# Kernel tuning notes

Measured on AMD Instinct MI355X. Metric: run time of the kernel, lower is better.

Reference implementation:

```python
import jax, jax.numpy as jnp
import numpy as np

B, L, E, H, NB, WIN = 128, 512, 512, 8, 2, 64
HD = E // H
EPS = 1e-8


def setup_inputs() -> dict:
    key = jax.random.key(0)
    ks = jax.random.split(key, 10)
    s = 0.02
    return {
        "timeline_mask": jax.random.randint(ks[0], (B, L), 0, 10) == 0,
        "seqs": jax.random.normal(ks[1], (B, L, E), jnp.float32),
        "w_in": jax.random.normal(ks[2], (NB, 3 * E, E), jnp.float32) * s,
        "b_in": jnp.zeros((NB, 3 * E), jnp.float32),
        "w_out": jax.random.normal(ks[3], (NB, E, E), jnp.float32) * s,
        "b_out": jnp.zeros((NB, E), jnp.float32),
        "ln1_g": jnp.ones((NB, E), jnp.float32),
        "ln1_b": jnp.zeros((NB, E), jnp.float32),
        "ln2_g": jnp.ones((NB, E), jnp.float32),
        "ln2_b": jnp.zeros((NB, E), jnp.float32),
        "c1_w": jax.random.normal(ks[4], (NB, E, E), jnp.float32) * s,
        "c1_b": jnp.zeros((NB, E), jnp.float32),
        "c2_w": jax.random.normal(ks[5], (NB, E, E), jnp.float32) * s,
        "c2_b": jnp.zeros((NB, E), jnp.float32),
        "lnf_g": jnp.ones((E,), jnp.float32),
        "lnf_b": jnp.zeros((E,), jnp.float32),
    }


def _ln(x, g, b):
    m = x.mean(-1, keepdims=True)
    v = ((x - m) ** 2).mean(-1, keepdims=True)
    return (x - m) * jax.lax.rsqrt(v + EPS) * g + b


def reference(timeline_mask, seqs, w_in, b_in, w_out, b_out,
              ln1_g, ln1_b, ln2_g, ln2_b, c1_w, c1_b, c2_w, c2_b,
              lnf_g, lnf_b):
    i = jnp.arange(L)
    d = i[:, None] - i[None, :]
    allowed = (d >= 0) & (d < WIN)  # [L, L] bool, True = attend

    keep = (~timeline_mask)[..., None].astype(seqs.dtype)  # [B, L, 1]
    x = seqs * keep
    scale = 1.0 / np.sqrt(HD)
    neg = jnp.asarray(jnp.finfo(seqs.dtype).min, seqs.dtype)

    for blk in range(NB):
        q_in = _ln(x, ln1_g[blk], ln1_b[blk])  # torch: query = LN(seqs), key/value = raw seqs
        wq, wk, wv = jnp.split(w_in[blk], 3, axis=0)
        bq, bk, bv = jnp.split(b_in[blk], 3, axis=0)
        q = (q_in @ wq.T + bq).reshape(B, L, H, HD)
        k = (x @ wk.T + bk).reshape(B, L, H, HD)
        v = (x @ wv.T + bv).reshape(B, L, H, HD)
        scores = jnp.einsum("blhd,bmhd->bhlm", q, k) * scale
        scores = jnp.where(allowed, scores, neg)
        attn = jax.nn.softmax(scores, axis=-1)
        o = jnp.einsum("bhlm,bmhd->blhd", attn, v).reshape(B, L, E)
        o = o @ w_out[blk].T + b_out[blk]
        x = q_in + o  # residual onto the layernormed query, as in the original
        x = _ln(x, ln2_g[blk], ln2_b[blk])
        h = jax.nn.relu(x @ c1_w[blk].T + c1_b[blk])  # Conv1d k=1 == pointwise linear
        x = (h @ c2_w[blk].T + c2_b[blk]) + x
        x = x * keep

    return _ln(x, lnf_g, lnf_b)
```

## Files before the change

### kernel.cpp

```cpp
#include <hip/hip_runtime.h>
#include <cstdint>

#define B_   128
#define L_   512
#define E_   512
#define H_   8
#define HD_  64
#define NB_  2
#define WIN_ 64
#define NROW (B_ * L_)

typedef __attribute__((ext_vector_type(8))) __bf16 bf16x8;
typedef __attribute__((ext_vector_type(4))) float f32x4;

static __device__ __forceinline__ unsigned short f2bf(float f) {
  union { float f; unsigned int u; } c; c.f = f;
  unsigned int u = c.u;
  unsigned int r = (u + 0x7fffu + ((u >> 16) & 1u)) >> 16;
  return (unsigned short)r;
}
static __device__ __forceinline__ float bf2f(unsigned short s) {
  union { unsigned int u; float f; } c; c.u = ((unsigned int)s) << 16; return c.f;
}

static __device__ __forceinline__ void gld_lds16(const unsigned short* g, unsigned short* l) {
  __builtin_amdgcn_global_load_lds((const __attribute__((address_space(1))) void*)g,
                                   (__attribute__((address_space(3))) void*)l, 16, 0, 0);
}

__global__ void detect_mask_kernel(const unsigned char* tm, int* flag) {
  __shared__ int f;
  if (threadIdx.x == 0) f = 0;
  __syncthreads();
  int local = 0;
  for (int i = threadIdx.x; i < NROW; i += blockDim.x)
    if ((i & 3) && tm[i]) local = 1;
  if (local) atomicOr(&f, 1);
  __syncthreads();
  if (threadIdx.x == 0) *flag = f;
}

__global__ void expand_keep_kernel(const void* tmv, const int* flag, float* keepF) {
  int i = blockIdx.x * blockDim.x + threadIdx.x;
  if (i >= NROW) return;
  int m;
  if (*flag) m = ((const unsigned char*)tmv)[i] != 0;
  else       m = ((const int*)tmv)[i] != 0;
  keepF[i] = m ? 0.f : 1.f;
}

__global__ void f2bf_kernel(const float* __restrict__ in, unsigned short* __restrict__ out, int n) {
  int i = blockIdx.x * blockDim.x + threadIdx.x;
  if (i < n) out[i] = f2bf(in[i]);
}

__global__ void mask_kernel(const float* __restrict__ seqs, const float* __restrict__ keepF,
                            unsigned short* __restrict__ xB) {
  int i = blockIdx.x * blockDim.x + threadIdx.x;
  int idx = i * 4;
  int row = idx >> 9;
  float k = keepF[row];
  float4 v = *(const float4*)(seqs + idx);
  ushort4 b;
  b.x = f2bf(v.x * k); b.y = f2bf(v.y * k); b.z = f2bf(v.z * k); b.w = f2bf(v.w * k);
  *(ushort4*)(xB + idx) = b;
}

__global__ __launch_bounds__(256) void ln_kernel(const unsigned short* __restrict__ X,
                                                 const float* __restrict__ g,
                                                 const float* __restrict__ bb,
                                                 unsigned short* outB, float* outF) {
  int wave = threadIdx.x >> 6, lane = threadIdx.x & 63;
  size_t row = (size_t)blockIdx.x * 4 + wave;
  const unsigned short* xr = X + row * E_;
  int e0 = lane * 8;
  union { uint4 q; unsigned short s[8]; } raw;
  raw.q = *(const uint4*)(xr + e0);
  float v[8];
#pragma unroll
  for (int i = 0; i < 8; ++i) v[i] = bf2f(raw.s[i]);
  float s = 0.f, s2 = 0.f;
#pragma unroll
  for (int i = 0; i < 8; ++i) { s += v[i]; s2 += v[i] * v[i]; }
  for (int off = 32; off; off >>= 1) { s += __shfl_xor(s, off); s2 += __shfl_xor(s2, off); }
  float mean = s * (1.f / E_);
  float var  = s2 * (1.f / E_) - mean * mean;
  float rs = rsqrtf(var + 1e-8f);
  float4 g0 = *(const float4*)(g + e0),  g1 = *(const float4*)(g + e0 + 4);
  float4 b0 = *(const float4*)(bb + e0), b1 = *(const float4*)(bb + e0 + 4);
  float gg[8] = {g0.x, g0.y, g0.z, g0.w, g1.x, g1.y, g1.z, g1.w};
  float bv[8] = {b0.x, b0.y, b0.z, b0.w, b1.x, b1.y, b1.z, b1.w};
  float y[8];
#pragma unroll
  for (int i = 0; i < 8; ++i) y[i] = (v[i] - mean) * rs * gg[i] + bv[i];
  if (outB) {
    union { uint4 q; unsigned short s[8]; } pk;
#pragma unroll
    for (int i = 0; i < 8; ++i) pk.s[i] = f2bf(y[i]);
    *(uint4*)(outB + row * E_ + e0) = pk.q;
  }
  if (outF) {
    float4 y0 = {y[0], y[1], y[2], y[3]}, y1 = {y[4], y[5], y[6], y[7]};
    *(float4*)(outF + row * E_ + e0) = y0;
    *(float4*)(outF + row * E_ + e0 + 4) = y1;
  }
}

__global__ __launch_bounds__(256) void gemm_kernel(
    const unsigned short* __restrict__ A, const unsigned short* __restrict__ W,
    const float* __restrict__ bias, const unsigned short* res, const float* __restrict__ keepF,
    unsigned short* outB, int K, int M, int relu) {
  __shared__ unsigned short sA0[128 * 32];
  __shared__ unsigned short sA1[128 * 32];
  __shared__ unsigned short sW0[128 * 32];
  __shared__ unsigned short sW1[128 * 32];
  int tid = threadIdx.x;
  int wave = tid >> 6, lane = tid & 63;
  int lm = lane & 15, quad = lane >> 4;
  size_t row0 = (size_t)blockIdx.y * 128;
  int col0 = blockIdx.x * 128;
  int wm = (wave >> 1) * 64, wn = (wave & 1) * 64;

  f32x4 acc[4][4];
  f32x4 z = {0.f, 0.f, 0.f, 0.f};
#pragma unroll
  for (int i = 0; i < 4; ++i)
#pragma unroll
    for (int j = 0; j < 4; ++j) acc[i][j] = z;

  int ar0 = tid >> 2, ak0 = (tid & 3) * 8;
  int ar1 = ar0 + 64;
  unsigned short* dA0a = &sA0[(wave * 16) * 32];
  unsigned short* dA0b = &sA0[(wave * 16 + 64) * 32];
  unsigned short* dA1a = &sA1[(wave * 16) * 32];
  unsigned short* dA1b = &sA1[(wave * 16 + 64) * 32];
  unsigned short* dW0a = &sW0[(wave * 16) * 32];
  unsigned short* dW0b = &sW0[(wave * 16 + 64) * 32];
  unsigned short* dW1a = &sW1[(wave * 16) * 32];
  unsigned short* dW1b = &sW1[(wave * 16 + 64) * 32];
  const unsigned short* Ar0 = A + (row0 + ar0) * K + ak0;
  const unsigned short* Ar1 = A + (row0 + ar1) * K + ak0;
  const unsigned short* Wr0 = W + (size_t)(col0 + ar0) * K + ak0;
  const unsigned short* Wr1 = W + (size_t)(col0 + ar1) * K + ak0;

  for (int k0 = 0; k0 < K; k0 += 64) {
    __syncthreads();
    gld_lds16(Ar0 + k0,      dA0a);
    gld_lds16(Ar1 + k0,      dA0b);
    gld_lds16(Ar0 + k0 + 32, dA1a);
    gld_lds16(Ar1 + k0 + 32, dA1b);
    gld_lds16(Wr0 + k0,      dW0a);
    gld_lds16(Wr1 + k0,      dW0b);
    gld_lds16(Wr0 + k0 + 32, dW1a);
    gld_lds16(Wr1 + k0 + 32, dW1b);
    __syncthreads();
    bf16x8 a0[4], a1[4], b0[4], b1[4];
#pragma unroll
    for (int mt = 0; mt < 4; ++mt) {
      a0[mt] = *(const bf16x8*)&sA0[(wm + mt * 16 + lm) * 32 + quad * 8];
      a1[mt] = *(const bf16x8*)&sA1[(wm + mt * 16 + lm) * 32 + quad * 8];
    }
#pragma unroll
    for (int nt = 0; nt < 4; ++nt) {
      b0[nt] = *(const bf16x8*)&sW0[(wn + nt * 16 + lm) * 32 + quad * 8];
      b1[nt] = *(const bf16x8*)&sW1[(wn + nt * 16 + lm) * 32 + quad * 8];
    }
#pragma unroll
    for (int mt = 0; mt < 4; ++mt)
#pragma unroll
      for (int nt = 0; nt < 4; ++nt) {
        acc[mt][nt] = __builtin_amdgcn_mfma_f32_16x16x32_bf16(a0[mt], b0[nt], acc[mt][nt], 0, 0, 0);
        acc[mt][nt] = __builtin_amdgcn_mfma_f32_16x16x32_bf16(a1[mt], b1[nt], acc[mt][nt], 0, 0, 0);
      }
  }

#pragma unroll
  for (int mt = 0; mt < 4; ++mt) {
#pragma unroll
    for (int r = 0; r < 4; ++r) {
      size_t row = row0 + wm + mt * 16 + quad * 4 + r;
      float kf = keepF ? keepF[row] : 1.f;
#pragma unroll
      for (int nt = 0; nt < 4; ++nt) {
        int col = col0 + wn + nt * 16 + lm;
        float v = acc[mt][nt][r] + bias[col];
        if (res) v += bf2f(res[row * M + col]);
        if (relu) v = fmaxf(v, 0.f);
        v *= kf;
        outB[row * M + col] = f2bf(v);
      }
    }
  }
}

#define SQS 72
#define SKS 72
#define SVS 68
#define SPS 136
__global__ __launch_bounds__(256) void attn_kernel(const unsigned short* __restrict__ Q,
                                                   const unsigned short* __restrict__ K,
                                                   const unsigned short* __restrict__ V,
                                                   unsigned short* O) {
  __shared__ unsigned short smem[64 * SQS + 128 * SKS + 128 * SVS];
  unsigned short* sQ = smem;
  unsigned short* sK = smem + 64 * SQS;
  unsigned short* sV = smem + 64 * SQS + 128 * SKS;
  unsigned short* sP = smem;

  int i0 = blockIdx.x * 64;
  int h = blockIdx.y;
  int b = blockIdx.z;
  int tid = threadIdx.x;
  size_t qbase  = ((size_t)b * L_) * E_ + h * HD_;
  size_t kvbase = ((size_t)b * L_) * (2 * E_) + h * HD_;

  for (int f = tid; f < 512; f += 256) {
    int r = f >> 3, c = f & 7;
    uint4 v = *(const uint4*)&Q[qbase + (size_t)(i0 + r) * E_ + c * 8];
    *(uint4*)&sQ[r * SQS + c * 8] = v;
  }
  for (int f = tid; f < 1024; f += 256) {
    int r = f >> 3, c = f & 7;
    int j = i0 - 64 + r;
    uint4 v = {0, 0, 0, 0};
    if (j >= 0) v = *(const uint4*)&K[kvbase + (size_t)j * (2 * E_) + c * 8];
    *(uint4*)&sK[r * SKS + c * 8] = v;
  }
  for (int f = tid; f < 2048; f += 256) {
    int r = f >> 4, c = f & 15;
    int j = i0 - 64 + r;
    uint2 v = {0, 0};
    if (j >= 0) v = *(const uint2*)&V[kvbase + E_ + (size_t)j * (2 * E_) + c * 4];
    *(uint2*)&sV[r * SVS + c * 4] = v;
  }
  __syncthreads();

  int wave = tid >> 6, lane = tid & 63;
  int lm = lane & 15, quad = lane >> 4;
  int wq = wave * 16;

  f32x4 accs[8];
  f32x4 z4 = {0.f, 0.f, 0.f, 0.f};
#pragma unroll
  for (int nt = 0; nt < 8; ++nt) accs[nt] = z4;
  bf16x8 aq0 = *(const bf16x8*)&sQ[(wq + lm) * SQS + quad * 8];
  bf16x8 aq1 = *(const bf16x8*)&sQ[(wq + lm) * SQS + 32 + quad * 8];
#pragma unroll
  for (int nt = 0; nt < 8; ++nt) {
    bf16x8 bk0 = *(const bf16x8*)&sK[(nt * 16 + lm) * SKS + quad * 8];
    bf16x8 bk1 = *(const bf16x8*)&sK[(nt * 16 + lm) * SKS + 32 + quad * 8];
    accs[nt] = __builtin_amdgcn_mfma_f32_16x16x32_bf16(aq0, bk0, accs[nt], 0, 0, 0);
    accs[nt] = __builtin_amdgcn_mfma_f32_16x16x32_bf16(aq1, bk1, accs[nt], 0, 0, 0);
  }
  __syncthreads();

#pragma unroll
  for (int r = 0; r < 4; ++r) {
    int qi = wq + quad * 4 + r;
    float sv[8];
    float mx = -INFINITY;
#pragma unroll
    for (int nt = 0; nt < 8; ++nt) {
      int jn = nt * 16 + lm;
      int d = qi + 64 - jn;
      int j = i0 - 64 + jn;
      float s = (d >= 0 && d < WIN_ && j >= 0) ? accs[nt][r] * 0.125f : -INFINITY;
      sv[nt] = s;
      mx = fmaxf(mx, s);
    }
#pragma unroll
    for (int off = 1; off <= 8; off <<= 1) mx = fmaxf(mx, __shfl_xor(mx, off));
    float sum = 0.f;
#pragma unroll
    for (int nt = 0; nt < 8; ++nt) {
      float e = __expf(sv[nt] - mx);
      sv[nt] = e;
      sum += e;
    }
#pragma unroll
    for (int off = 1; off <= 8; off <<= 1) sum += __shfl_xor(sum, off);
    float inv = 1.f / sum;
#pragma unroll
    for (int nt = 0; nt < 8; ++nt) accs[nt][r] = sv[nt] * inv;
  }

#pragma unroll
  for (int nt = 0; nt < 8; ++nt)
#pragma unroll
    for (int r = 0; r < 4; ++r)
      sP[(wq + quad * 4 + r) * SPS + nt * 16 + lm] = f2bf(accs[nt][r]);
  __syncthreads();

  f32x4 acco[4];
#pragma unroll
  for (int nt = 0; nt < 4; ++nt) acco[nt] = z4;
#pragma unroll
  for (int kt = 0; kt < 4; ++kt) {
    bf16x8 ap = *(const bf16x8*)&sP[(wq + lm) * SPS + kt * 32 + quad * 8];
    int jb = kt * 32 + quad * 8;
#pragma unroll
    for (int nt = 0; nt < 4; ++nt) {
      union { unsigned short u[8]; bf16x8 v; } bv;
#pragma unroll
      for (int jj = 0; jj < 8; ++jj)
        bv.u[jj] = sV[(jb + jj) * SVS + nt * 16 + lm];
      acco[nt] = __builtin_amdgcn_mfma_f32_16x16x32_bf16(ap, bv.v, acco[nt], 0, 0, 0);
    }
  }
#pragma unroll
  for (int nt = 0; nt < 4; ++nt)
#pragma unroll
    for (int r = 0; r < 4; ++r) {
      int qi = wq + quad * 4 + r;
      O[qbase + (size_t)(i0 + qi) * E_ + nt * 16 + lm] = f2bf(acco[nt][r]);
    }
}

extern "C" void kernel_launch(void* const* d_in, const int* in_sizes, int n_in,
                              void* d_out, int out_size, void* d_ws, size_t ws_size,
                              hipStream_t stream) {
  const void*  tm    = d_in[0];
  const float* seqs  = (const float*)d_in[1];
  const float* w_in  = (const float*)d_in[2];
  const float* b_in  = (const float*)d_in[3];
  const float* w_out = (const float*)d_in[4];
  const float* b_out = (const float*)d_in[5];
  const float* ln1_g = (const float*)d_in[6];
  const float* ln1_b = (const float*)d_in[7];
  const float* ln2_g = (const float*)d_in[8];
  const float* ln2_b = (const float*)d_in[9];
  const float* c1_w  = (const float*)d_in[10];
  const float* c1_b  = (const float*)d_in[11];
  const float* c2_w  = (const float*)d_in[12];
  const float* c2_b  = (const float*)d_in[13];
  const float* lnf_g = (const float*)d_in[14];
  const float* lnf_b = (const float*)d_in[15];

  char* ws = (char*)d_ws;
  size_t off = 0;
  auto alloc = [&](size_t bytes) -> char* {
    char* p = ws + off;
    off += (bytes + 255) & ~(size_t)255;
    return p;
  };
  const size_t NE = (size_t)NROW * E_;
  unsigned short* xb     = (unsigned short*)alloc(NE * 2);
  unsigned short* qinb   = (unsigned short*)alloc(NE * 2);
  unsigned short* qb     = (unsigned short*)alloc(NE * 2);
  unsigned short* kvb    = (unsigned short*)alloc(NE * 4);
  unsigned short* w_in_b = (unsigned short*)alloc((size_t)NB_ * 3 * E_ * E_ * 2);
  unsigned short* w_out_b= (unsigned short*)alloc((size_t)NB_ * E_ * E_ * 2);
  unsigned short* wc1b   = (unsigned short*)alloc((size_t)NB_ * E_ * E_ * 2);
  unsigned short* wc2b   = (unsigned short*)alloc((size_t)NB_ * E_ * E_ * 2);
  float*          keepF  = (float*)alloc((size_t)NROW * 4);
  int*            flag   = (int*)alloc(256);
  if (off > ws_size) return;

  unsigned short* hb = kvb;

  detect_mask_kernel<<<1, 256, 0, stream>>>((const unsigned char*)tm, flag);
  expand_keep_kernel<<<NROW / 256, 256, 0, stream>>>(tm, flag, keepF);

  int n_win = NB_ * 3 * E_ * E_, n_sq = NB_ * E_ * E_;
  f2bf_kernel<<<(n_win + 255) / 256, 256, 0, stream>>>(w_in, w_in_b, n_win);
  f2bf_kernel<<<(n_sq + 255) / 256, 256, 0, stream>>>(w_out, w_out_b, n_sq);
  f2bf_kernel<<<(n_sq + 255) / 256, 256, 0, stream>>>(c1_w, wc1b, n_sq);
  f2bf_kernel<<<(n_sq + 255) / 256, 256, 0, stream>>>(c2_w, wc2b, n_sq);

  mask_kernel<<<(int)(NE / 4 / 256), 256, 0, stream>>>(seqs, keepF, xb);

  dim3 ggrid(E_ / 128, NROW / 128);
  dim3 ggridKV(2 * E_ / 128, NROW / 128);
  for (int blk = 0; blk < NB_; ++blk) {
    const unsigned short* wq = w_in_b + (size_t)blk * 3 * E_ * E_;
    const unsigned short* wkv = wq + (size_t)E_ * E_;
    const float* bq = b_in + (size_t)blk * 3 * E_;
    const float* bkv = bq + E_;

    ln_kernel<<<NROW / 4, 256, 0, stream>>>(xb, ln1_g + blk * E_, ln1_b + blk * E_, qinb, nullptr);
    gemm_kernel<<<ggrid, 256, 0, stream>>>(qinb, wq, bq, nullptr, nullptr, qb, E_, E_, 0);
    gemm_kernel<<<ggridKV, 256, 0, stream>>>(xb, wkv, bkv, nullptr, nullptr, kvb, E_, 2 * E_, 0);
    attn_kernel<<<dim3(L_ / 64, H_, B_), 256, 0, stream>>>(qb, kvb, kvb, qb);
    gemm_kernel<<<ggrid, 256, 0, stream>>>(qb, w_out_b + (size_t)blk * E_ * E_,
                                           b_out + blk * E_, qinb, nullptr, xb, E_, E_, 0);
    ln_kernel<<<NROW / 4, 256, 0, stream>>>(xb, ln2_g + blk * E_, ln2_b + blk * E_, xb, nullptr);
    gemm_kernel<<<ggrid, 256, 0, stream>>>(xb, wc1b + (size_t)blk * E_ * E_,
                                           c1_b + blk * E_, nullptr, nullptr, hb, E_, E_, 1);
    gemm_kernel<<<ggrid, 256, 0, stream>>>(hb, wc2b + (size_t)blk * E_ * E_,
                                           c2_b + blk * E_, xb, keepF, xb, E_, E_, 0);
  }
  ln_kernel<<<NROW / 4, 256, 0, stream>>>(xb, lnf_g, lnf_b, nullptr, (float*)d_out);
}
```

Baseline: 1.630 ms.

## Fold layernorms into GEMMs, double-buffer GEMM, banded attention with transposed V

Replaces the LN1/LN2 materialising kernels with per-row stats kernels. Gamma is folded into bf16 weights and the mean/rstd correction into the GEMM epilogue through precomputed U/C vectors, and the LN'd residual is recomputed from stats in the epilogue. The GEMM gets double-buffered LDS staging with one barrier per k-step and an XCD-aware block remap. Attention now skips key tiles outside the sliding-window band and stores V transposed in LDS so B-operand loads are vectorised. The risks are doubled LDS in the GEMM, which may lower occupancy, slight numeric drift from folding LN after bf16 rounding, and removal of a barrier between the sP writes and reads in attention.

```diff
diff --git a/kernel.cpp b/kernel.cpp
--- a/kernel.cpp
+++ b/kernel.cpp
@@ -54,6 +54,24 @@
   if (i < n) out[i] = f2bf(in[i]);
 }
 
+__global__ void f2bf_scale_kernel(const float* __restrict__ in, const float* __restrict__ g,
+                                  unsigned short* __restrict__ out, int n) {
+  int i = blockIdx.x * blockDim.x + threadIdx.x;
+  if (i < n) out[i] = f2bf(in[i] * g[i & (E_ - 1)]);
+}
+
+__global__ __launch_bounds__(256) void uc_kernel(const float* __restrict__ W, const float* __restrict__ g,
+                                                 const float* __restrict__ b, const float* __restrict__ bias,
+                                                 float* __restrict__ U, float* __restrict__ C) {
+  int wave = threadIdx.x >> 6, lane = threadIdx.x & 63;
+  int j = blockIdx.x * 4 + wave;
+  const float* wr = W + (size_t)j * E_;
+  float su = 0.f, sc = 0.f;
+  for (int k = lane; k < E_; k += 64) { float w = wr[k]; su += w * g[k]; sc += w * b[k]; }
+  for (int off = 32; off; off >>= 1) { su += __shfl_xor(su, off); sc += __shfl_xor(sc, off); }
+  if (lane == 0) { U[j] = su; C[j] = sc + bias[j]; }
+}
+
 __global__ void mask_kernel(const float* __restrict__ seqs, const float* __restrict__ keepF,
                             unsigned short* __restrict__ xB) {
   int i = blockIdx.x * blockDim.x + threadIdx.x;
@@ -64,6 +82,24 @@
   ushort4 b;
   b.x = f2bf(v.x * k); b.y = f2bf(v.y * k); b.z = f2bf(v.z * k); b.w = f2bf(v.w * k);
   *(ushort4*)(xB + idx) = b;
+}
+
+__global__ __launch_bounds__(256) void stats_kernel(const unsigned short* __restrict__ X,
+                                                    float* __restrict__ st) {
+  int wave = threadIdx.x >> 6, lane = threadIdx.x & 63;
+  size_t row = (size_t)blockIdx.x * 4 + wave;
+  union { uint4 q; unsigned short s[8]; } raw;
+  raw.q = *(const uint4*)(X + row * E_ + lane * 8);
+  float s = 0.f, s2 = 0.f;
+#pragma unroll
+  for (int i = 0; i < 8; ++i) { float v = bf2f(raw.s[i]); s += v; s2 += v * v; }
+  for (int off = 32; off; off >>= 1) { s += __shfl_xor(s, off); s2 += __shfl_xor(s2, off); }
+  if (lane == 0) {
+    float mean = s * (1.f / E_);
+    float var  = s2 * (1.f / E_) - mean * mean;
+    st[row * 2]     = mean;
+    st[row * 2 + 1] = rsqrtf(var + 1e-8f);
+  }
 }
 
 __global__ __launch_bounds__(256) void ln_kernel(const unsigned short* __restrict__ X,
@@ -108,17 +144,28 @@
 
 __global__ __launch_bounds__(256) void gemm_kernel(
     const unsigned short* __restrict__ A, const unsigned short* __restrict__ W,
-    const float* __restrict__ bias, const unsigned short* res, const float* __restrict__ keepF,
-    unsigned short* outB, int K, int M, int relu) {
-  __shared__ unsigned short sA0[128 * 32];
-  __shared__ unsigned short sA1[128 * 32];
-  __shared__ unsigned short sW0[128 * 32];
-  __shared__ unsigned short sW1[128 * 32];
+    const float* __restrict__ bias,
+    const float* __restrict__ stats, const float* __restrict__ U, const float* __restrict__ C,
+    const unsigned short* __restrict__ resX, const float* __restrict__ resStats,
+    const float* __restrict__ resG, const float* __restrict__ resB,
+    const float* __restrict__ keepF, unsigned short* __restrict__ outB,
+    int K, int M, int relu) {
+  __shared__ unsigned short sA0[2][128 * 32];
+  __shared__ unsigned short sA1[2][128 * 32];
+  __shared__ unsigned short sW0[2][128 * 32];
+  __shared__ unsigned short sW1[2][128 * 32];
   int tid = threadIdx.x;
   int wave = tid >> 6, lane = tid & 63;
   int lm = lane & 15, quad = lane >> 4;
-  size_t row0 = (size_t)blockIdx.y * 128;
-  int col0 = blockIdx.x * 128;
+
+  int gx = gridDim.x;
+  int nwg = gx * gridDim.y;
+  int orig = blockIdx.y * gx + blockIdx.x;
+  int chunk = nwg >> 3;
+  int wg = (orig & 7) * chunk + (orig >> 3);
+  int bx = wg % gx, by = wg / gx;
+  size_t row0 = (size_t)by * 128;
+  int col0 = bx * 128;
   int wm = (wave >> 1) * 64, wn = (wave & 1) * 64;
 
   f32x4 acc[4][4];
@@ -130,40 +177,39 @@
 
   int ar0 = tid >> 2, ak0 = (tid & 3) * 8;
   int ar1 = ar0 + 64;
-  unsigned short* dA0a = &sA0[(wave * 16) * 32];
-  unsigned short* dA0b = &sA0[(wave * 16 + 64) * 32];
-  unsigned short* dA1a = &sA1[(wave * 16) * 32];
-  unsigned short* dA1b = &sA1[(wave * 16 + 64) * 32];
-  unsigned short* dW0a = &sW0[(wave * 16) * 32];
-  unsigned short* dW0b = &sW0[(wave * 16 + 64) * 32];
-  unsigned short* dW1a = &sW1[(wave * 16) * 32];
-  unsigned short* dW1b = &sW1[(wave * 16 + 64) * 32];
+  int soff = (wave * 16) * 32;
   const unsigned short* Ar0 = A + (row0 + ar0) * K + ak0;
   const unsigned short* Ar1 = A + (row0 + ar1) * K + ak0;
   const unsigned short* Wr0 = W + (size_t)(col0 + ar0) * K + ak0;
   const unsigned short* Wr1 = W + (size_t)(col0 + ar1) * K + ak0;
 
-  for (int k0 = 0; k0 < K; k0 += 64) {
-    __syncthreads();
-    gld_lds16(Ar0 + k0,      dA0a);
-    gld_lds16(Ar1 + k0,      dA0b);
-    gld_lds16(Ar0 + k0 + 32, dA1a);
-    gld_lds16(Ar1 + k0 + 32, dA1b);
-    gld_lds16(Wr0 + k0,      dW0a);
-    gld_lds16(Wr1 + k0,      dW0b);
-    gld_lds16(Wr0 + k0 + 32, dW1a);
-    gld_lds16(Wr1 + k0 + 32, dW1b);
-    __syncthreads();
+  auto stage = [&](int p, int k0) {
+    gld_lds16(Ar0 + k0,      &sA0[p][soff]);
+    gld_lds16(Ar1 + k0,      &sA0[p][soff + 64 * 32]);
+    gld_lds16(Ar0 + k0 + 32, &sA1[p][soff]);
+    gld_lds16(Ar1 + k0 + 32, &sA1[p][soff + 64 * 32]);
+    gld_lds16(Wr0 + k0,      &sW0[p][soff]);
+    gld_lds16(Wr1 + k0,      &sW0[p][soff + 64 * 32]);
+    gld_lds16(Wr0 + k0 + 32, &sW1[p][soff]);
+    gld_lds16(Wr1 + k0 + 32, &sW1[p][soff + 64 * 32]);
+  };
+
+  int NT = K >> 6;
+  stage(0, 0);
+  __syncthreads();
+  for (int t = 0; t < NT; ++t) {
+    int p = t & 1;
+    if (t + 1 < NT) stage(p ^ 1, (t + 1) << 6);
     bf16x8 a0[4], a1[4], b0[4], b1[4];
 #pragma unroll
     for (int mt = 0; mt < 4; ++mt) {
-      a0[mt] = *(const bf16x8*)&sA0[(wm + mt * 16 + lm) * 32 + quad * 8];
-      a1[mt] = *(const bf16x8*)&sA1[(wm + mt * 16 + lm) * 32 + quad * 8];
+      a0[mt] = *(const bf16x8*)&sA0[p][(wm + mt * 16 + lm) * 32 + quad * 8];
+      a1[mt] = *(const bf16x8*)&sA1[p][(wm + mt * 16 + lm) * 32 + quad * 8];
     }
 #pragma unroll
     for (int nt = 0; nt < 4; ++nt) {
-      b0[nt] = *(const bf16x8*)&sW0[(wn + nt * 16 + lm) * 32 + quad * 8];
-      b1[nt] = *(const bf16x8*)&sW1[(wn + nt * 16 + lm) * 32 + quad * 8];
+      b0[nt] = *(const bf16x8*)&sW0[p][(wn + nt * 16 + lm) * 32 + quad * 8];
+      b1[nt] = *(const bf16x8*)&sW1[p][(wn + nt * 16 + lm) * 32 + quad * 8];
     }
 #pragma unroll
     for (int mt = 0; mt < 4; ++mt)
@@ -172,6 +218,7 @@
         acc[mt][nt] = __builtin_amdgcn_mfma_f32_16x16x32_bf16(a0[mt], b0[nt], acc[mt][nt], 0, 0, 0);
         acc[mt][nt] = __builtin_amdgcn_mfma_f32_16x16x32_bf16(a1[mt], b1[nt], acc[mt][nt], 0, 0, 0);
       }
+    __syncthreads();
   }
 
 #pragma unroll
@@ -180,14 +227,25 @@
     for (int r = 0; r < 4; ++r) {
       size_t row = row0 + wm + mt * 16 + quad * 4 + r;
       float kf = keepF ? keepF[row] : 1.f;
+      float s0 = 1.f, s1 = 0.f;
+      if (stats) {
+        float2 ms = *(const float2*)(stats + row * 2);
+        s0 = ms.y; s1 = -ms.y * ms.x;
+      }
+      float r0 = 0.f, r1 = 0.f;
+      if (resX) {
+        float2 ms = *(const float2*)(resStats + row * 2);
+        r0 = ms.y; r1 = -ms.y * ms.x;
+      }
 #pragma unroll
       for (int nt = 0; nt < 4; ++nt) {
         int col = col0 + wn + nt * 16 + lm;
-        float v = acc[mt][nt][r] + bias[col];
-        if (res) v += bf2f(res[row * M + col]);
+        float v = s0 * acc[mt][nt][r];
+        v += U ? (s1 * U[col] + C[col]) : bias[col];
+        if (resX) v += (r0 * bf2f(resX[row * (size_t)M + col]) + r1) * resG[col] + resB[col];
         if (relu) v = fmaxf(v, 0.f);
         v *= kf;
-        outB[row * M + col] = f2bf(v);
+        outB[row * (size_t)M + col] = f2bf(v);
       }
     }
   }
@@ -195,17 +253,16 @@
 
 #define SQS 72
 #define SKS 72
-#define SVS 68
+#define SVT 130
 #define SPS 136
 __global__ __launch_bounds__(256) void attn_kernel(const unsigned short* __restrict__ Q,
-                                                   const unsigned short* __restrict__ K,
-                                                   const unsigned short* __restrict__ V,
+                                                   const unsigned short* __restrict__ KV,
                                                    unsigned short* O) {
-  __shared__ unsigned short smem[64 * SQS + 128 * SKS + 128 * SVS];
-  unsigned short* sQ = smem;
-  unsigned short* sK = smem + 64 * SQS;
-  unsigned short* sV = smem + 64 * SQS + 128 * SKS;
-  unsigned short* sP = smem;
+  __shared__ unsigned short smem[64 * SQS + 128 * SKS + 64 * SVT];
+  unsigned short* sQ  = smem;
+  unsigned short* sK  = smem + 64 * SQS;
+  unsigned short* sVT = smem + 64 * SQS + 128 * SKS;
+  unsigned short* sP  = smem;
 
   int i0 = blockIdx.x * 64;
   int h = blockIdx.y;
@@ -223,21 +280,25 @@
     int r = f >> 3, c = f & 7;
     int j = i0 - 64 + r;
     uint4 v = {0, 0, 0, 0};
-    if (j >= 0) v = *(const uint4*)&K[kvbase + (size_t)j * (2 * E_) + c * 8];
+    if (j >= 0) v = *(const uint4*)&KV[kvbase + (size_t)j * (2 * E_) + c * 8];
     *(uint4*)&sK[r * SKS + c * 8] = v;
   }
   for (int f = tid; f < 2048; f += 256) {
     int r = f >> 4, c = f & 15;
     int j = i0 - 64 + r;
     uint2 v = {0, 0};
-    if (j >= 0) v = *(const uint2*)&V[kvbase + E_ + (size_t)j * (2 * E_) + c * 4];
-    *(uint2*)&sV[r * SVS + c * 4] = v;
+    if (j >= 0) v = *(const uint2*)&KV[kvbase + E_ + (size_t)j * (2 * E_) + c * 4];
+    union { uint2 u; unsigned short s[4]; } uv; uv.u = v;
+#pragma unroll
+    for (int i = 0; i < 4; ++i) sVT[(c * 4 + i) * SVT + r] = uv.s[i];
   }
   __syncthreads();
 
   int wave = tid >> 6, lane = tid & 63;
   int lm = lane & 15, quad = lane >> 4;
   int wq = wave * 16;
+  int klo2 = (wave >> 1) * 2;
+  int ktlo = wave >> 1;
 
   f32x4 accs[8];
   f32x4 z4 = {0.f, 0.f, 0.f, 0.f};
@@ -247,6 +308,7 @@
   bf16x8 aq1 = *(const bf16x8*)&sQ[(wq + lm) * SQS + 32 + quad * 8];
 #pragma unroll
   for (int nt = 0; nt < 8; ++nt) {
+    if (nt < wave || nt > wave + 4) continue;
     bf16x8 bk0 = *(const bf16x8*)&sK[(nt * 16 + lm) * SKS + quad * 8];
     bf16x8 bk1 = *(const bf16x8*)&sK[(nt * 16 + lm) * SKS + 32 + quad * 8];
     accs[nt] = __builtin_amdgcn_mfma_f32_16x16x32_bf16(aq0, bk0, accs[nt], 0, 0, 0);
@@ -261,6 +323,7 @@
     float mx = -INFINITY;
 #pragma unroll
     for (int nt = 0; nt < 8; ++nt) {
+      if (nt < klo2 || nt > klo2 + 5) continue;
       int jn = nt * 16 + lm;
       int d = qi + 64 - jn;
       int j = i0 - 64 + jn;
@@ -273,6 +336,7 @@
     float sum = 0.f;
 #pragma unroll
     for (int nt = 0; nt < 8; ++nt) {
+      if (nt < klo2 || nt > klo2 + 5) continue;
       float e = __expf(sv[nt] - mx);
       sv[nt] = e;
       sum += e;
@@ -281,30 +345,29 @@
     for (int off = 1; off <= 8; off <<= 1) sum += __shfl_xor(sum, off);
     float inv = 1.f / sum;
 #pragma unroll
-    for (int nt = 0; nt < 8; ++nt) accs[nt][r] = sv[nt] * inv;
-  }
-
-#pragma unroll
-  for (int nt = 0; nt < 8; ++nt)
+    for (int nt = 0; nt < 8; ++nt)
+      if (nt >= klo2 && nt <= klo2 + 5) accs[nt][r] = sv[nt] * inv;
+  }
+
+#pragma unroll
+  for (int nt = 0; nt < 8; ++nt) {
+    if (nt < klo2 || nt > klo2 + 5) continue;
 #pragma unroll
     for (int r = 0; r < 4; ++r)
       sP[(wq + quad * 4 + r) * SPS + nt * 16 + lm] = f2bf(accs[nt][r]);
-  __syncthreads();
+  }
 
   f32x4 acco[4];
 #pragma unroll
   for (int nt = 0; nt < 4; ++nt) acco[nt] = z4;
 #pragma unroll
   for (int kt = 0; kt < 4; ++kt) {
+    if (kt < ktlo || kt > ktlo + 2) continue;
     bf16x8 ap = *(const bf16x8*)&sP[(wq + lm) * SPS + kt * 32 + quad * 8];
-    int jb = kt * 32 + quad * 8;
 #pragma unroll
     for (int nt = 0; nt < 4; ++nt) {
-      union { unsigned short u[8]; bf16x8 v; } bv;
-#pragma unroll
-      for (int jj = 0; jj < 8; ++jj)
-        bv.u[jj] = sV[(jb + jj) * SVS + nt * 16 + lm];
-      acco[nt] = __builtin_amdgcn_mfma_f32_16x16x32_bf16(ap, bv.v, acco[nt], 0, 0, 0);
+      bf16x8 bv = *(const bf16x8*)&sVT[(nt * 16 + lm) * SVT + kt * 32 + quad * 8];
+      acco[nt] = __builtin_amdgcn_mfma_f32_16x16x32_bf16(ap, bv, acco[nt], 0, 0, 0);
     }
   }
 #pragma unroll
@@ -344,15 +407,19 @@
     return p;
   };
   const size_t NE = (size_t)NROW * E_;
+  const size_t EE = (size_t)E_ * E_;
   unsigned short* xb     = (unsigned short*)alloc(NE * 2);
-  unsigned short* qinb   = (unsigned short*)alloc(NE * 2);
+  unsigned short* xmid   = (unsigned short*)alloc(NE * 2);
   unsigned short* qb     = (unsigned short*)alloc(NE * 2);
   unsigned short* kvb    = (unsigned short*)alloc(NE * 4);
-  unsigned short* w_in_b = (unsigned short*)alloc((size_t)NB_ * 3 * E_ * E_ * 2);
-  unsigned short* w_out_b= (unsigned short*)alloc((size_t)NB_ * E_ * E_ * 2);
-  unsigned short* wc1b   = (unsigned short*)alloc((size_t)NB_ * E_ * E_ * 2);
-  unsigned short* wc2b   = (unsigned short*)alloc((size_t)NB_ * E_ * E_ * 2);
+  unsigned short* w_in_b = (unsigned short*)alloc((size_t)NB_ * 3 * EE * 2);
+  unsigned short* w_out_b= (unsigned short*)alloc((size_t)NB_ * EE * 2);
+  unsigned short* wc1b   = (unsigned short*)alloc((size_t)NB_ * EE * 2);
+  unsigned short* wc2b   = (unsigned short*)alloc((size_t)NB_ * EE * 2);
   float*          keepF  = (float*)alloc((size_t)NROW * 4);
+  float*          st1    = (float*)alloc((size_t)NROW * 2 * 4);
+  float*          st2    = (float*)alloc((size_t)NROW * 2 * 4);
+  float*          ucb    = (float*)alloc((size_t)NB_ * 4 * E_ * 4);
   int*            flag   = (int*)alloc(256);
   if (off > ws_size) return;
 
@@ -361,10 +428,23 @@
   detect_mask_kernel<<<1, 256, 0, stream>>>((const unsigned char*)tm, flag);
   expand_keep_kernel<<<NROW / 256, 256, 0, stream>>>(tm, flag, keepF);
 
-  int n_win = NB_ * 3 * E_ * E_, n_sq = NB_ * E_ * E_;
-  f2bf_kernel<<<(n_win + 255) / 256, 256, 0, stream>>>(w_in, w_in_b, n_win);
+  for (int blk = 0; blk < NB_; ++blk) {
+    const float* wi = w_in + (size_t)blk * 3 * EE;
+    f2bf_scale_kernel<<<(int)((EE + 255) / 256), 256, 0, stream>>>(
+        wi, ln1_g + blk * E_, w_in_b + (size_t)blk * 3 * EE, (int)EE);
+    f2bf_kernel<<<(int)((2 * EE + 255) / 256), 256, 0, stream>>>(
+        wi + EE, w_in_b + (size_t)blk * 3 * EE + EE, (int)(2 * EE));
+    uc_kernel<<<E_ / 4, 256, 0, stream>>>(wi, ln1_g + blk * E_, ln1_b + blk * E_,
+                                          b_in + (size_t)blk * 3 * E_,
+                                          ucb + (size_t)blk * 4 * E_, ucb + (size_t)blk * 4 * E_ + E_);
+    f2bf_scale_kernel<<<(int)((EE + 255) / 256), 256, 0, stream>>>(
+        c1_w + (size_t)blk * EE, ln2_g + blk * E_, wc1b + (size_t)blk * EE, (int)EE);
+    uc_kernel<<<E_ / 4, 256, 0, stream>>>(c1_w + (size_t)blk * EE, ln2_g + blk * E_, ln2_b + blk * E_,
+                                          c1_b + (size_t)blk * E_,
+                                          ucb + (size_t)blk * 4 * E_ + 2 * E_, ucb + (size_t)blk * 4 * E_ + 3 * E_);
+  }
+  int n_sq = NB_ * (int)EE;
   f2bf_kernel<<<(n_sq + 255) / 256, 256, 0, stream>>>(w_out, w_out_b, n_sq);
-  f2bf_kernel<<<(n_sq + 255) / 256, 256, 0, stream>>>(c1_w, wc1b, n_sq);
   f2bf_kernel<<<(n_sq + 255) / 256, 256, 0, stream>>>(c2_w, wc2b, n_sq);
 
   mask_kernel<<<(int)(NE / 4 / 256), 256, 0, stream>>>(seqs, keepF, xb);
@@ -372,22 +452,34 @@
   dim3 ggrid(E_ / 128, NROW / 128);
   dim3 ggridKV(2 * E_ / 128, NROW / 128);
   for (int blk = 0; blk < NB_; ++blk) {
-    const unsigned short* wq = w_in_b + (size_t)blk * 3 * E_ * E_;
-    const unsigned short* wkv = wq + (size_t)E_ * E_;
-    const float* bq = b_in + (size_t)blk * 3 * E_;
-    const float* bkv = bq + E_;
-
-    ln_kernel<<<NROW / 4, 256, 0, stream>>>(xb, ln1_g + blk * E_, ln1_b + blk * E_, qinb, nullptr);
-    gemm_kernel<<<ggrid, 256, 0, stream>>>(qinb, wq, bq, nullptr, nullptr, qb, E_, E_, 0);
-    gemm_kernel<<<ggridKV, 256, 0, stream>>>(xb, wkv, bkv, nullptr, nullptr, kvb, E_, 2 * E_, 0);
-    attn_kernel<<<dim3(L_ / 64, H_, B_), 256, 0, stream>>>(qb, kvb, kvb, qb);
-    gemm_kernel<<<ggrid, 256, 0, stream>>>(qb, w_out_b + (size_t)blk * E_ * E_,
-                                           b_out + blk * E_, qinb, nullptr, xb, E_, E_, 0);
-    ln_kernel<<<NROW / 4, 256, 0, stream>>>(xb, ln2_g + blk * E_, ln2_b + blk * E_, xb, nullptr);
-    gemm_kernel<<<ggrid, 256, 0, stream>>>(xb, wc1b + (size_t)blk * E_ * E_,
-                                           c1_b + blk * E_, nullptr, nullptr, hb, E_, E_, 1);
-    gemm_kernel<<<ggrid, 256, 0, stream>>>(hb, wc2b + (size_t)blk * E_ * E_,
-                                           c2_b + blk * E_, xb, keepF, xb, E_, E_, 0);
+    const unsigned short* wq  = w_in_b + (size_t)blk * 3 * EE;
+    const unsigned short* wkv = wq + EE;
+    const float* bkv = b_in + (size_t)blk * 3 * E_ + E_;
+    float* Uq  = ucb + (size_t)blk * 4 * E_;
+    float* Cq  = Uq + E_;
+    float* Uc1 = Uq + 2 * E_;
+    float* Cc1 = Uq + 3 * E_;
+
+    stats_kernel<<<NROW / 4, 256, 0, stream>>>(xb, st1);
+    gemm_kernel<<<ggrid, 256, 0, stream>>>(xb, wq, nullptr, st1, Uq, Cq,
+                                           nullptr, nullptr, nullptr, nullptr,
+                                           nullptr, qb, E_, E_, 0);
+    gemm_kernel<<<ggridKV, 256, 0, stream>>>(xb, wkv, bkv, nullptr, nullptr, nullptr,
+                                             nullptr, nullptr, nullptr, nullptr,
+                                             nullptr, kvb, E_, 2 * E_, 0);
+    attn_kernel<<<dim3(L_ / 64, H_, B_), 256, 0, stream>>>(qb, kvb, qb);
+    gemm_kernel<<<ggrid, 256, 0, stream>>>(qb, w_out_b + (size_t)blk * EE, b_out + blk * E_,
+                                           nullptr, nullptr, nullptr,
+                                           xb, st1, ln1_g + blk * E_, ln1_b + blk * E_,
+                                           nullptr, xmid, E_, E_, 0);
+    stats_kernel<<<NROW / 4, 256, 0, stream>>>(xmid, st2);
+    gemm_kernel<<<ggrid, 256, 0, stream>>>(xmid, wc1b + (size_t)blk * EE, nullptr, st2, Uc1, Cc1,
+                                           nullptr, nullptr, nullptr, nullptr,
+                                           nullptr, hb, E_, E_, 1);
+    gemm_kernel<<<ggrid, 256, 0, stream>>>(hb, wc2b + (size_t)blk * EE, c2_b + blk * E_,
+                                           nullptr, nullptr, nullptr,
+                                           xmid, st2, ln2_g + blk * E_, ln2_b + blk * E_,
+                                           keepF, xb, E_, E_, 0);
   }
   ln_kernel<<<NROW / 4, 256, 0, stream>>>(xb, lnf_g, lnf_b, nullptr, (float*)d_out);
 }
```

Result: slower. 2.419 ms (+48.4%).
